# Optimization experiments

Hardware: AMD Instinct MI355X
Metric: run time of the kernel (lower is better)

The kernel has to match this reference:

```python
import jax, jax.numpy as jnp
import numpy as np

DEPTH = 4
H1 = 64
H2 = 16
NF = 5
L = 10.0
K = 4
DIM = 3
N = 2048
NK = N // 4
FEAT = 1 + 2 * NF * DIM  # r scalar + Nf (cos,sin) pairs of dim components


def _tn(k, shape, std=0.01):
    return jax.random.truncated_normal(k, -2.0, 2.0, shape, jnp.float32) * std


def setup_inputs() -> dict:
    key = jax.random.key(0)
    ks = jax.random.split(key, 16)
    comb0 = 3 * DIM + 3 * FEAT   # combine width at depth 0
    combd = 3 * H1 + 3 * H2      # combine width at later depths
    return {
        "sx": jax.random.uniform(ks[0], (N, DIM), jnp.float32) * L,
        "kpoints": jax.random.normal(ks[1], (2 * NK, DIM), jnp.float32),
        "we0": _tn(ks[2], (comb0, H1)), "be0": jnp.zeros((H1,), jnp.float32),
        "we_rest": _tn(ks[3], (DEPTH - 1, combd, H1)), "be_rest": jnp.zeros((DEPTH - 1, H1), jnp.float32),
        "wee0": _tn(ks[4], (FEAT, H2)), "bee0": jnp.zeros((H2,), jnp.float32),
        "wee_rest": _tn(ks[5], (DEPTH - 2, H2, H2)), "bee_rest": jnp.zeros((DEPTH - 2, H2), jnp.float32),
        "wep0": _tn(ks[6], (FEAT, H2)), "bep0": jnp.zeros((H2,), jnp.float32),
        "wep_rest": _tn(ks[7], (DEPTH - 2, H2, H2)), "bep_rest": jnp.zeros((DEPTH - 2, H2), jnp.float32),
        "orb_w_re": _tn(ks[8], (H1, H1)), "orb_w_im": _tn(ks[9], (H1, H1)),
        "orb_b_re": jnp.zeros((H1,), jnp.float32), "orb_b_im": jnp.zeros((H1,), jnp.float32),
        "w_det": _tn(ks[10], (K, H1, H1)),
        "bf_w": _tn(ks[11], (H1, DIM)),
        "mlp_w1": _tn(ks[12], (DIM, H1)), "mlp_b1": jnp.zeros((H1,), jnp.float32),
        "mlp_w2": _tn(ks[13], (H1, K * (NK - 1))), "mlp_b2": jnp.zeros((K * (NK - 1),), jnp.float32),
    }


def _fourier(rij, r):
    # interleaved [r, cos1, sin1, ..., cosNf, sinNf] like the original
    feats = [r[..., None]]
    for k in range(1, NF + 1):
        ang = (2.0 * np.pi * k / L) * rij
        feats.append(jnp.cos(ang))
        feats.append(jnp.sin(ang))
    return jnp.concatenate(feats, axis=-1)


def _combine(e, ee, ep):
    mm = e.shape[0]
    h = mm // 2
    g1a = jnp.broadcast_to(jnp.mean(e[:h], 0, keepdims=True), e.shape)
    g1b = jnp.broadcast_to(jnp.mean(e[h:], 0, keepdims=True), e.shape)
    g2a = jnp.mean(ee[:h], axis=0)
    g2b = jnp.mean(ee[h:], axis=0)
    g3 = jnp.mean(ep, axis=1)
    return jnp.concatenate([e, g1a, g1b, g2a, g2b, g3], axis=1)


def _forward(sx, kpoints, we0, be0, we_rest, be_rest, wee0, bee0, wee_rest, bee_rest,
             wep0, bep0, wep_rest, bep_rest, orb_w_re, orb_w_im, orb_b_re, orb_b_im,
             w_det, bf_w, mlp_w1, mlp_b1, mlp_w2, mlp_b2):
    n, dim = sx.shape
    m, m2 = n // 2, n // 4
    s, x = sx[:m], sx[m:]
    e = jnp.broadcast_to(kpoints[0][None, :], (m, dim))
    # electron-electron pairwise features (m,m,FEAT)
    rij = x[:, None, :] - x[None, :, :]
    eye = jnp.eye(m, dtype=x.dtype)
    r = jnp.linalg.norm(jnp.sin(np.pi * rij / L) + eye[..., None], axis=-1) * (1.0 - eye) * (L / np.pi)
    ee = _fourier(rij, r)
    # electron-proton pairwise features (m,m,FEAT)
    rij = x[:, None, :] - s[None, :, :]
    r = jnp.linalg.norm(jnp.sin(np.pi * rij / L), axis=-1) * (L / np.pi)
    ep = _fourier(rij, r)
    for d in range(DEPTH - 1):
        f = _combine(e, ee, ep)
        We, be = (we0, be0) if d == 0 else (we_rest[d - 1], be_rest[d - 1])
        Wee, bee = (wee0, bee0) if d == 0 else (wee_rest[d - 1], bee_rest[d - 1])
        Wep, bep = (wep0, bep0) if d == 0 else (wep_rest[d - 1], bep_rest[d - 1])
        e_u = jnp.tanh(f @ We + be)
        ee_u = jnp.tanh(ee @ Wee + bee)
        ep_u = jnp.tanh(ep @ Wep + bep)
        e, ee, ep = (e_u + e, ee_u + ee, ep_u + ep) if d > 0 else (e_u, ee_u, ep_u)
    f = _combine(e, ee, ep)
    e = jnp.tanh(f @ we_rest[-1] + be_rest[-1]) + e
    # complex orbitals and geminal pairing matrix phi: (K, m2, m2)
    orb = e.astype(jnp.complex64) @ (orb_w_re + 1j * orb_w_im) + (orb_b_re + 1j * orb_b_im)
    phi = jnp.einsum('ia,kab,jb->kij', orb[:m2], w_det.astype(jnp.complex64), orb[m2:]) + 1.0
    # backflow coordinates and plane-wave determinant factors
    z = e @ bf_w + x
    nk = kpoints.shape[0] // 2
    norm = 1.0 / L ** (dim / 2)
    D_up = norm * jnp.exp(1j * jnp.einsum('kd,id->ki', kpoints[:nk], z[:m2]))  # (nk, m2)
    D_dn = norm * jnp.exp(1j * jnp.einsum('kd,id->ki', kpoints[nk:], z[m2:]))  # (nk, m2)
    h = jnp.tanh(kpoints[0] @ mlp_w1 + mlp_b1)
    fdet = jax.nn.softplus(h @ mlp_w2 + mlp_b2).reshape(K, nk - 1)
    fdet = jnp.concatenate([jnp.ones((K, 1), fdet.dtype), fdet], axis=1)  # (K, nk)
    D = jnp.einsum('ai,ka,aj->kij', D_up, fdet.astype(D_up.dtype), jnp.conj(D_dn))
    # logdet_matmul: stable log of signed sum of K determinants
    phase, logabs = jnp.linalg.slogdet(D * phi)
    maxl = jnp.max(logabs)
    det = jnp.sum(phase * jnp.exp(logabs - maxl))
    return jnp.log(jnp.abs(det)) + maxl + jnp.log(det / jnp.abs(det))


def reference(sx, kpoints, we0, be0, we_rest, be_rest, wee0, bee0, wee_rest, bee_rest,
              wep0, bep0, wep_rest, bep_rest, orb_w_re, orb_w_im, orb_b_re, orb_b_im,
              w_det, bf_w, mlp_w1, mlp_b1, mlp_w2, mlp_b2):
    return _forward(sx, kpoints, we0, be0, we_rest, be_rest, wee0, bee0, wee_rest, bee_rest,
                    wep0, bep0, wep_rest, bep_rest, orb_w_re, orb_w_im, orb_b_re, orb_b_im,
                    w_det, bf_w, mlp_w1, mlp_b1, mlp_w2, mlp_b2)
```

## Files before the change

kernel.cpp:

```cpp
#include <hip/hip_runtime.h>

typedef unsigned int uint;
typedef unsigned short ushort;

#define M1 1024
#define MH 512
#define PI_F 3.14159265358979323846f
#define LBOX 10.0f
#define NB 32

__device__ __forceinline__ float bf2f(ushort h){ return __uint_as_float(((uint)h)<<16); }
__device__ __forceinline__ ushort f2bf(float f){ uint u = __float_as_uint(f); uint r = (u + 0x7fffu + ((u>>16)&1u))>>16; return (ushort)r; }
__device__ __forceinline__ float ftanh(float x){ float e = __expf(2.f*x); return 1.f - 2.f/(e+1.f); }
__device__ __forceinline__ float2 cmul(float2 a, float2 b){ return make_float2(a.x*b.x - a.y*b.y, a.x*b.y + a.y*b.x); }
__device__ __forceinline__ void cfma(float2& c, float2 a, float2 b){
  c.x = fmaf(a.x,b.x,fmaf(-a.y,b.y,c.x));
  c.y = fmaf(a.x,b.y,fmaf(a.y,b.x,c.y));
}

__device__ __forceinline__ void fourier31(float d0, float d1, float d2, bool diag, float f[31]){
  const float k1 = PI_F / LBOX;
  float s[3], c[3];
  __sincosf(k1*d0, &s[0], &c[0]);
  __sincosf(k1*d1, &s[1], &c[1]);
  __sincosf(k1*d2, &s[2], &c[2]);
  float r = diag ? 0.f : (LBOX/PI_F)*sqrtf(s[0]*s[0]+s[1]*s[1]+s[2]*s[2]);
  f[0] = r;
  float cb[3], sb[3], cc[3], sc[3];
  #pragma unroll
  for (int d=0; d<3; ++d){ cb[d] = 1.f - 2.f*s[d]*s[d]; sb[d] = 2.f*s[d]*c[d]; cc[d]=cb[d]; sc[d]=sb[d]; }
  #pragma unroll
  for (int k=0;k<5;++k){
    #pragma unroll
    for (int d=0; d<3; ++d){ f[1+6*k+d] = cc[d]; f[4+6*k+d] = sc[d]; }
    if (k<4){
      #pragma unroll
      for (int d=0; d<3; ++d){
        float nc = cc[d]*cb[d]-sc[d]*sb[d];
        float ns = sc[d]*cb[d]+cc[d]*sb[d];
        cc[d]=nc; sc[d]=ns;
      }
    }
  }
}

__global__ void k_init(float* __restrict__ p, int n, int* __restrict__ rowmap){
  int i = blockIdx.x*256 + threadIdx.x;
  if (i < 2048) rowmap[i] = i & 511;
  for (int q=i; q<n; q+=gridDim.x*256) p[q] = 0.f;
}

__global__ __launch_bounds__(256) void k_pair0(const float* __restrict__ sx, const float* __restrict__ W,
                                               const float* __restrict__ b, ushort* __restrict__ out, int is_ee,
                                               float* __restrict__ gA, float* __restrict__ gB,
                                               float* __restrict__ gH){
  int bx = blockIdx.x;
  int i = bx >> 2;
  int chunk = bx & 3;
  int j = (chunk << 8) + threadIdx.x;
  const float* xs = sx + 3*M1;
  float xi0 = xs[3*i], xi1 = xs[3*i+1], xi2 = xs[3*i+2];
  const float* oth = is_ee ? xs : sx;
  float y0 = oth[3*j], y1 = oth[3*j+1], y2 = oth[3*j+2];
  float f[31];
  fourier31(xi0-y0, xi1-y1, xi2-y2, is_ee && (i==j), f);
  float acc[16];
  #pragma unroll
  for (int o=0;o<16;++o) acc[o] = b[o];
  #pragma unroll
  for (int c=0;c<31;++c){ float fv = f[c];
    #pragma unroll
    for (int o=0;o<16;++o) acc[o] = fmaf(fv, W[c*16+o], acc[o]);
  }
  float hv[16];
  #pragma unroll
  for (int o=0;o<16;++o) hv[o] = ftanh(acc[o]);
  uint u[8];
  #pragma unroll
  for (int h=0;h<8;++h){
    u[h] = (uint)f2bf(hv[2*h]) | ((uint)f2bf(hv[2*h+1])<<16);
  }
  uint4* dst = (uint4*)(out + ((size_t)i*M1 + j)*16);
  dst[0] = make_uint4(u[0],u[1],u[2],u[3]);
  dst[1] = make_uint4(u[4],u[5],u[6],u[7]);
  __shared__ float buf[256*49];
  #pragma unroll
  for (int c=0;c<31;++c) buf[threadIdx.x*49+c] = f[c];
  #pragma unroll
  for (int c=0;c<16;++c) buf[threadIdx.x*49+31+c] = hv[c];
  __syncthreads();
  #pragma unroll
  for (int s=128; s>0; s>>=1){
    if (threadIdx.x < s){
      #pragma unroll
      for (int c=0;c<47;++c) buf[threadIdx.x*49+c] += buf[(threadIdx.x+s)*49+c];
    }
    __syncthreads();
  }
  if (threadIdx.x < 31){
    float* g = (is_ee && chunk >= 2) ? gB : gA;
    atomicAdd(&g[i*31+threadIdx.x], buf[threadIdx.x]);
  } else if (threadIdx.x < 47 && gH){
    atomicAdd(&gH[i*16 + (threadIdx.x-31)], buf[threadIdx.x]);
  }
}

__global__ __launch_bounds__(256) void k_pairU(ushort* __restrict__ ten, const float* __restrict__ W,
                                               const float* __restrict__ b, float* __restrict__ gOut){
  size_t base = ((size_t)blockIdx.x*256 + threadIdx.x)*16;
  uint4 a0 = ((uint4*)(ten+base))[0];
  uint4 a1 = ((uint4*)(ten+base))[1];
  uint uu[8] = {a0.x,a0.y,a0.z,a0.w,a1.x,a1.y,a1.z,a1.w};
  float v[16];
  #pragma unroll
  for (int h=0;h<8;++h){ v[2*h] = bf2f((ushort)(uu[h]&0xffffu)); v[2*h+1] = bf2f((ushort)(uu[h]>>16)); }
  float acc[16];
  #pragma unroll
  for (int o=0;o<16;++o) acc[o] = b[o];
  #pragma unroll
  for (int c=0;c<16;++c){ float fv = v[c];
    #pragma unroll
    for (int o=0;o<16;++o) acc[o] = fmaf(fv, W[c*16+o], acc[o]);
  }
  float nv[16];
  #pragma unroll
  for (int o=0;o<16;++o) nv[o] = ftanh(acc[o]) + v[o];
  uint w[8];
  #pragma unroll
  for (int h=0;h<8;++h){
    w[h] = (uint)f2bf(nv[2*h]) | ((uint)f2bf(nv[2*h+1])<<16);
  }
  ((uint4*)(ten+base))[0] = make_uint4(w[0],w[1],w[2],w[3]);
  ((uint4*)(ten+base))[1] = make_uint4(w[4],w[5],w[6],w[7]);
  __shared__ float buf[256*17];
  if (gOut){
    #pragma unroll
    for (int c=0;c<16;++c) buf[threadIdx.x*17+c] = nv[c];
    __syncthreads();
    #pragma unroll
    for (int s=128; s>0; s>>=1){
      if (threadIdx.x < s){
        #pragma unroll
        for (int c=0;c<16;++c) buf[threadIdx.x*17+c] += buf[(threadIdx.x+s)*17+c];
      }
      __syncthreads();
    }
    if (threadIdx.x < 16){
      int i = blockIdx.x >> 2;
      atomicAdd(&gOut[i*16 + threadIdx.x], buf[threadIdx.x]);
    }
  }
}

__global__ __launch_bounds__(256) void k_gee(const ushort* __restrict__ ten, float* __restrict__ gA, float* __restrict__ gB){
  int jb = blockIdx.x >> 3;
  int ic = blockIdx.x & 7;
  int jl = threadIdx.x & 63;
  int iq = threadIdx.x >> 6;
  int j = jb*64 + jl;
  float acc[16];
  #pragma unroll
  for (int c=0;c<16;++c) acc[c]=0.f;
  for (int s=0;s<32;++s){
    int i = ic*128 + iq + 4*s;
    const uint4* src = (const uint4*)(ten + ((size_t)i*M1 + j)*16);
    uint4 a0 = src[0], a1 = src[1];
    uint uu[8]={a0.x,a0.y,a0.z,a0.w,a1.x,a1.y,a1.z,a1.w};
    #pragma unroll
    for (int h=0;h<8;++h){ acc[2*h]+=bf2f((ushort)(uu[h]&0xffffu)); acc[2*h+1]+=bf2f((ushort)(uu[h]>>16)); }
  }
  __shared__ float red[4][64][16];
  #pragma unroll
  for (int c=0;c<16;++c) red[iq][jl][c]=acc[c];
  __syncthreads();
  if (iq==0){
    float* out = (ic<4)? gA : gB;
    #pragma unroll
    for (int c=0;c<16;++c){
      float t = red[0][jl][c]+red[1][jl][c]+red[2][jl][c]+red[3][jl][c];
      atomicAdd(&out[j*16+c], t);
    }
  }
}

__global__ __launch_bounds__(256) void k_e0(const float* __restrict__ kp, const float* __restrict__ g2a,
    const float* __restrict__ g2b, const float* __restrict__ g3, const float* __restrict__ W,
    const float* __restrict__ b, float* __restrict__ eout, float* __restrict__ g1out){
  int p = blockIdx.x*4 + (threadIdx.x>>6);
  int o = threadIdx.x & 63;
  float acc = b[o];
  #pragma unroll
  for (int d=0; d<3; ++d){
    acc = fmaf(kp[d], W[d*64+o] + W[(d+3)*64+o] + W[(d+6)*64+o], acc);
  }
  const float i512 = 1.f/512.f, i1024 = 1.f/1024.f;
  #pragma unroll
  for (int c=0;c<31;++c){
    float sg = (c!=0 && ((c-1)%6)>=3) ? -i512 : i512;
    acc = fmaf(g2a[p*31+c]*sg, W[(9+c)*64+o], acc);
  }
  #pragma unroll
  for (int c=0;c<31;++c){
    float sg = (c!=0 && ((c-1)%6)>=3) ? -i512 : i512;
    acc = fmaf(g2b[p*31+c]*sg, W[(40+c)*64+o], acc);
  }
  #pragma unroll
  for (int c=0;c<31;++c) acc = fmaf(g3[p*31+c]*i1024, W[(71+c)*64+o], acc);
  float v = ftanh(acc);
  eout[p*64+o] = v;
  atomicAdd(&g1out[(p<MH?0:64)+o], v);
}

__global__ __launch_bounds__(256) void k_eupd(const float* __restrict__ eprev, float* __restrict__ eout,
    const float* __restrict__ W, const float* __restrict__ b, const float* __restrict__ g1in,
    const float* __restrict__ g2a, const float* __restrict__ g2b, const float* __restrict__ g3,
    float* __restrict__ g1out){
  int p = blockIdx.x*4 + (threadIdx.x>>6);
  int o = threadIdx.x & 63;
  const float i512 = 1.f/512.f, i1024 = 1.f/1024.f;
  float acc = b[o];
  #pragma unroll 8
  for (int c=0;c<64;++c) acc = fmaf(eprev[p*64+c], W[c*64+o], acc);
  #pragma unroll 8
  for (int c=0;c<64;++c) acc = fmaf(g1in[c]*i512, W[(64+c)*64+o], acc);
  #pragma unroll 8
  for (int c=0;c<64;++c) acc = fmaf(g1in[64+c]*i512, W[(128+c)*64+o], acc);
  #pragma unroll
  for (int c=0;c<16;++c) acc = fmaf(g2a[p*16+c]*i512, W[(192+c)*64+o], acc);
  #pragma unroll
  for (int c=0;c<16;++c) acc = fmaf(g2b[p*16+c]*i512, W[(208+c)*64+o], acc);
  #pragma unroll
  for (int c=0;c<16;++c) acc = fmaf(g3[p*16+c]*i1024, W[(224+c)*64+o], acc);
  float v = ftanh(acc) + eprev[p*64+o];
  eout[p*64+o] = v;
  if (g1out) atomicAdd(&g1out[(p<MH?0:64)+o], v);
}

__global__ __launch_bounds__(256) void k_orbz(const float* __restrict__ e4, const float* __restrict__ Wre,
    const float* __restrict__ Wim, const float* __restrict__ bre, const float* __restrict__ bim,
    const float* __restrict__ bfw, const float* __restrict__ sx, float* __restrict__ ore,
    float* __restrict__ oim, float* __restrict__ z){
  int p = blockIdx.x*4 + (threadIdx.x>>6);
  int o = threadIdx.x & 63;
  float ar = bre[o], ai = bim[o];
  #pragma unroll 8
  for (int a=0;a<64;++a){ float ev = e4[p*64+a]; ar = fmaf(ev, Wre[a*64+o], ar); ai = fmaf(ev, Wim[a*64+o], ai); }
  ore[p*64+o]=ar; oim[p*64+o]=ai;
  if (o<3){
    float zz = sx[(M1+p)*3+o];
    for (int a=0;a<64;++a) zz = fmaf(e4[p*64+a], bfw[a*3+o], zz);
    z[p*3+o]=zz;
  }
}

__global__ __launch_bounds__(256) void k_fdet(const float* __restrict__ kp, const float* __restrict__ w1,
    const float* __restrict__ b1, const float* __restrict__ w2, const float* __restrict__ b2,
    float* __restrict__ fdet){
  __shared__ float hs[64];
  int tid = threadIdx.x;
  if (tid < 64){
    float acc = b1[tid];
    for (int d=0;d<3;++d) acc = fmaf(kp[d], w1[d*64+tid], acc);
    hs[tid] = ftanh(acc);
  }
  __syncthreads();
  int c = blockIdx.x*256 + tid;
  if (c < 2044){
    float acc = b2[c];
    #pragma unroll 8
    for (int o=0;o<64;++o) acc = fmaf(hs[o], w2[o*2044+c], acc);
    float sp = (acc > 20.f) ? acc : log1pf(__expf(acc));
    int kk = c / 511, idx = c % 511;
    fdet[kk*512 + 1 + idx] = sp;
  }
  if (blockIdx.x == 0 && tid < 4) fdet[tid*512] = 1.f;
}

__global__ __launch_bounds__(256) void k_uv(const float* __restrict__ kp, const float* __restrict__ z,
                                            float2* __restrict__ U, float2* __restrict__ V){
  int gid = blockIdx.x*256 + threadIdx.x;
  int sel = gid >> 18;
  int rem = gid & 262143;
  int a = rem >> 9;
  int col = rem & 511;
  const float nrm = 0.031622776601683794f;
  const float* kr = kp + (sel ? (512+a)*3 : a*3);
  const float* zr = z + (sel ? (512+col)*3 : col*3);
  float th = kr[0]*zr[0] + kr[1]*zr[1] + kr[2]*zr[2];
  float s, c; __sincosf(th, &s, &c);
  float2 v = make_float2(nrm*c, nrm*s);
  if (sel) V[a*512+col] = v; else U[a*512+col] = v;
}

__global__ __launch_bounds__(256) void k_T(const float* __restrict__ ore, const float* __restrict__ oim,
                                           const float* __restrict__ wdet, float2* __restrict__ T){
  int k = blockIdx.x >> 7;
  int iblk = blockIdx.x & 127;
  int i = iblk*4 + (threadIdx.x>>6);
  int bc = threadIdx.x & 63;
  __shared__ float wd[4096];
  for (int t = threadIdx.x; t < 4096; t += 256) wd[t] = wdet[k*4096 + t];
  __syncthreads();
  float ar=0.f, ai=0.f;
  #pragma unroll 8
  for (int a=0;a<64;++a){
    float w = wd[a*64+bc];
    ar = fmaf(ore[i*64+a], w, ar);
    ai = fmaf(oim[i*64+a], w, ai);
  }
  T[((size_t)k*512 + i)*64 + bc] = make_float2(ar, ai);
}

__global__ __launch_bounds__(256) void k_M(const float2* __restrict__ U, const float2* __restrict__ V,
    const float* __restrict__ fdet, const float2* __restrict__ T, const float* __restrict__ ore,
    const float* __restrict__ oim, float2* __restrict__ Mb){
  __shared__ float2 As[16*66];
  __shared__ float2 Bs[16*66];
  int k = blockIdx.z;
  int ib = blockIdx.y * 64, jb = blockIdx.x * 64;
  int tid = threadIdx.x;
  int ti = (tid >> 4) * 4;
  int tj = (tid & 15) * 4;
  const float* fk = fdet + k*512;
  float2 acc[4][4];
  #pragma unroll
  for (int a=0;a<4;++a){
    #pragma unroll
    for (int b=0;b<4;++b) acc[a][b] = make_float2(0.f,0.f);
  }
  for (int a0=0; a0<512; a0+=16){
    #pragma unroll
    for (int s=0;s<4;++s){
      int t = tid + s*256;
      int aa = t >> 6, il = t & 63;
      int a = a0 + aa;
      float fv = fk[a];
      float2 u = U[a*512 + ib + il];
      As[aa*66+il] = make_float2(u.x*fv, u.y*fv);
      float2 v = V[a*512 + jb + il];
      Bs[aa*66+il] = make_float2(v.x, -v.y);
    }
    __syncthreads();
    #pragma unroll
    for (int aa=0;aa<16;++aa){
      float2 Av[4], Bv[4];
      #pragma unroll
      for (int q=0;q<4;++q){ Av[q] = As[aa*66+ti+q]; Bv[q] = Bs[aa*66+tj+q]; }
      #pragma unroll
      for (int qi=0;qi<4;++qi){
        #pragma unroll
        for (int qj=0;qj<4;++qj) cfma(acc[qi][qj], Av[qi], Bv[qj]);
      }
    }
    __syncthreads();
  }
  float2 ph[4][4];
  #pragma unroll
  for (int a=0;a<4;++a){
    #pragma unroll
    for (int b=0;b<4;++b) ph[a][b] = make_float2(1.f,0.f);
  }
  for (int b0=0; b0<64; b0+=16){
    #pragma unroll
    for (int s=0;s<4;++s){
      int t = tid + s*256;
      int aa = t >> 6, il = t & 63;
      As[aa*66+il] = T[((size_t)k*512 + ib + il)*64 + b0 + aa];
      int oidx = (512 + jb + il)*64 + b0 + aa;
      Bs[aa*66+il] = make_float2(ore[oidx], oim[oidx]);
    }
    __syncthreads();
    #pragma unroll
    for (int aa=0;aa<16;++aa){
      float2 Av[4], Bv[4];
      #pragma unroll
      for (int q=0;q<4;++q){ Av[q] = As[aa*66+ti+q]; Bv[q] = Bs[aa*66+tj+q]; }
      #pragma unroll
      for (int qi=0;qi<4;++qi){
        #pragma unroll
        for (int qj=0;qj<4;++qj) cfma(ph[qi][qj], Av[qi], Bv[qj]);
      }
    }
    __syncthreads();
  }
  #pragma unroll
  for (int qi=0;qi<4;++qi){
    size_t ro = ((size_t)k*512 + ib + ti + qi)*512 + jb + tj;
    #pragma unroll
    for (int qj=0;qj<4;++qj) Mb[ro+qj] = cmul(acc[qi][qj], ph[qi][qj]);
  }
}

__global__ __launch_bounds__(512)
void k_panel(float2* __restrict__ Mb, float2* __restrict__ LinvG,
             int* __restrict__ rowmap, int* __restrict__ swapc, int col0){
  int k = blockIdx.x;
  float2* Mk = Mb + (size_t)k*512*512;
  int R = 512 - col0;
  int R64 = R < 64 ? R : 64;
  int rl = threadIdx.x;
  bool active = rl < R;
  int wv = rl >> 6;
  __shared__ float2 mir[64*33];
  __shared__ float2 Us[NB*33];
  __shared__ float2 dinv[NB];
  __shared__ float2 Ls[NB*NB];
  __shared__ float2 Yv[NB*NB];
  __shared__ int winslot[NB];
  __shared__ int newposS[64];
  int rm_orig = active ? rowmap[k*512 + col0 + rl] : 0;
  float2 X[NB];
  if (rl >= 64 && active){
    const float4* rp = (const float4*)(Mk + (size_t)rm_orig*512 + col0);
    #pragma unroll
    for (int q=0;q<NB/2;++q){ float4 v = rp[q]; X[2*q]=make_float2(v.x,v.y); X[2*q+1]=make_float2(v.z,v.w); }
  }
  if (wv == 0){
    if (rl < R64){
      const float4* rp = (const float4*)(Mk + (size_t)rm_orig*512 + col0);
      #pragma unroll
      for (int q=0;q<NB/2;++q){
        float4 v = rp[q];
        mir[rl*33+2*q]   = make_float2(v.x,v.y);
        mir[rl*33+2*q+1] = make_float2(v.z,v.w);
      }
    }
    bool done = false;
    int winpos = 0;
    for (int cc=0; cc<NB; ++cc){
      bool cand = (rl < R64) && !done;
      float2 cv = make_float2(0.f,0.f);
      if (cand) cv = mir[rl*33+cc];
      float val = cand ? fmaf(cv.x,cv.x,cv.y*cv.y) : -1.f;
      int idx = rl;
      #pragma unroll
      for (int off=32; off>0; off>>=1){
        float ov = __shfl_xor(val, off);
        int   oi = __shfl_xor(idx, off);
        if (ov > val || (ov == val && oi < idx)){ val = ov; idx = oi; }
      }
      int p = idx;
      if (rl == 0) winslot[cc] = p;
      if (rl == p){ done = true; winpos = cc; }
      float2 dg = mir[p*33+cc];
      float dn = 1.f/fmaf(dg.x,dg.x,dg.y*dg.y);
      float2 inv = make_float2(dg.x*dn, -dg.y*dn);
      if (cand && rl != p){
        float2 l = cmul(cv, inv);
        mir[rl*33+cc] = l;
        for (int j=cc+1; j<NB; ++j){
          float2 pr = mir[p*33+j];
          float2 xv = mir[rl*33+j];
          xv.x = fmaf(-l.x, pr.x, fmaf( l.y, pr.y, xv.x));
          xv.y = fmaf(-l.x, pr.y, fmaf(-l.y, pr.x, xv.y));
          mir[rl*33+j] = xv;
        }
      }
    }
    unsigned long long nwmask = __ballot(rl < R64 && !done);
    int np = 0;
    if (rl < R64){
      np = done ? winpos : (NB + (int)__popcll(nwmask & ((1ull<<rl)-1ull)));
      newposS[rl] = np;
      rowmap[k*512 + col0 + np] = rm_orig;
      float4* wp = (float4*)(Mk + (size_t)rm_orig*512 + col0);
      #pragma unroll
      for (int q=0;q<NB/2;++q){
        float2 a = mir[rl*33+2*q], bq = mir[rl*33+2*q+1];
        wp[q] = make_float4(a.x,a.y,bq.x,bq.y);
      }
    }
    {
      int cnt = 0;
      for (int t=0;t<R64;++t){
        int nt = newposS[t];
        if (rl < R64 && t > rl && nt < np) cnt++;
      }
      #pragma unroll
      for (int off=32; off>0; off>>=1) cnt += __shfl_xor(cnt, off);
      if (rl == 0) swapc[k] += cnt;
    }
    if (rl < NB){
      int ws = winslot[rl];
      #pragma unroll
      for (int j=0;j<NB;++j){
        float2 v = mir[ws*33+j];
        Us[rl*33+j] = v;
        float2 lv;
        if      (j <  rl) lv = v;
        else if (j == rl) lv = make_float2(1.f,0.f);
        else              lv = make_float2(0.f,0.f);
        Ls[rl*NB+j] = lv;
      }
      float2 d = Us[rl*33+rl];
      float dn = 1.f/fmaf(d.x,d.x,d.y*d.y);
      dinv[rl] = make_float2(d.x*dn, -d.y*dn);
    }
  }
  __syncthreads();
  if (rl >= 64 && active){
    #pragma unroll
    for (int j=0;j<NB;++j){
      float2 t = X[j];
      #pragma unroll
      for (int q=0;q<NB;++q){
        if (q < j){
          float2 u = Us[q*33+j];
          t.x = fmaf(-X[q].x, u.x, fmaf( X[q].y, u.y, t.x));
          t.y = fmaf(-X[q].x, u.y, fmaf(-X[q].y, u.x, t.y));
        }
      }
      X[j] = cmul(t, dinv[j]);
    }
    float4* wp = (float4*)(Mk + (size_t)rm_orig*512 + col0);
    #pragma unroll
    for (int q=0;q<NB/2;++q) wp[q] = make_float4(X[2*q].x,X[2*q].y,X[2*q+1].x,X[2*q+1].y);
  }
  if (rl < NB){
    for (int i=0;i<NB;++i){
      float2 acc = (i==rl)? make_float2(1.f,0.f) : make_float2(0.f,0.f);
      for (int q=rl; q<i; ++q){
        float2 lv = Ls[i*NB+q];
        float2 yv = Yv[q*NB+rl];
        acc.x = fmaf(-lv.x, yv.x, fmaf( lv.y, yv.y, acc.x));
        acc.y = fmaf(-lv.x, yv.y, fmaf(-lv.y, yv.x, acc.y));
      }
      Yv[i*NB+rl] = acc;
    }
  }
  __syncthreads();
  {
    float4* dst = (float4*)(LinvG + (size_t)k*(NB*NB));
    const float4* src = (const float4*)Yv;
    for (int q=rl; q<NB*NB/2; q+=blockDim.x) dst[q] = src[q];
  }
}

__global__ __launch_bounds__(256) void k_gemm(float2* __restrict__ Mb, const float2* __restrict__ LinvG,
                                              const int* __restrict__ rowmap, int col0){
  int k = blockIdx.z;
  float2* Mk = Mb + (size_t)k*512*512;
  int e0 = col0 + NB;
  int r0 = e0 + blockIdx.x*32;
  int j0c = e0 + blockIdx.y*32;
  int tid = threadIdx.x;
  int jl = tid & 31, rg = tid >> 5;
  __shared__ float2 As[NB*33];
  __shared__ float2 Bs[NB*33];
  __shared__ float2 Av[NB*33];
  __shared__ float2 Li[NB*NB];
  __shared__ int prA[32];
  __shared__ int prB[NB];
  if (tid < 32) prA[tid] = rowmap[k*512 + r0 + tid];
  else if (tid < 64) prB[tid-32] = rowmap[k*512 + col0 + (tid-32)];
  {
    const float4* src = (const float4*)(LinvG + (size_t)k*(NB*NB));
    float4* dst = (float4*)Li;
    for (int q=tid; q<NB*NB/2; q+=256) dst[q] = src[q];
  }
  __syncthreads();
  #pragma unroll
  for (int s=0;s<4;++s){
    int a = rg + 8*s;
    Av[a*33 + jl] = Mk[(size_t)prB[a]*512 + j0c + jl];
  }
  for (int t=tid; t<1024; t+=256){
    int rl = t >> 5, kk = t & 31;
    As[kk*33+rl] = Mk[(size_t)prA[rl]*512 + col0 + kk];
  }
  __syncthreads();
  #pragma unroll
  for (int s=0;s<4;++s){
    int m = rg + 8*s;
    float2 acc = make_float2(0.f,0.f);
    #pragma unroll 8
    for (int a=0;a<NB;++a) cfma(acc, Li[m*NB+a], Av[a*33+jl]);
    Bs[m*33+jl] = acc;
  }
  __syncthreads();
  int i0 = (tid >> 4)*2, j0 = (tid & 15)*2;
  float2 a00={0,0},a01={0,0},a10={0,0},a11={0,0};
  #pragma unroll 16
  for (int kk=0;kk<NB;++kk){
    float2 A0 = As[kk*33+i0], A1 = As[kk*33+i0+1];
    float2 B0 = Bs[kk*33+j0], B1 = Bs[kk*33+j0+1];
    cfma(a00,A0,B0); cfma(a01,A0,B1); cfma(a10,A1,B0); cfma(a11,A1,B1);
  }
  size_t ro0 = (size_t)prA[i0]*512 + j0c + j0;
  size_t ro1 = (size_t)prA[i0+1]*512 + j0c + j0;
  float2 c0 = Mk[ro0];   c0.x-=a00.x; c0.y-=a00.y; Mk[ro0]=c0;
  float2 c1 = Mk[ro0+1]; c1.x-=a01.x; c1.y-=a01.y; Mk[ro0+1]=c1;
  float2 c2 = Mk[ro1];   c2.x-=a10.x; c2.y-=a10.y; Mk[ro1]=c2;
  float2 c3 = Mk[ro1+1]; c3.x-=a11.x; c3.y-=a11.y; Mk[ro1+1]=c3;
}

__global__ void k_det(const float2* __restrict__ Mb, const int* __restrict__ rowmap,
                      const int* __restrict__ swapc, float* __restrict__ out, int out_size){
  int tid = threadIdx.x;
  int k = tid >> 6, lane = tid & 63;
  const float2* Mk = Mb + (size_t)k*512*512;
  double la = 0.0, ang = 0.0;
  for (int q=0;q<8;++q){
    int i = lane*8 + q;
    int pr = rowmap[k*512 + i];
    float2 u = Mk[(size_t)pr*512+i];
    double re = (double)u.x, im = (double)u.y;
    la += 0.5*log(re*re + im*im);
    ang += atan2(im, re);
  }
  #pragma unroll
  for (int off=32; off>0; off>>=1){
    la += __shfl_down(la, off);
    ang += __shfl_down(ang, off);
  }
  __shared__ double las[4], angs[4];
  if (lane==0){
    las[k] = la;
    angs[k] = ang + 3.14159265358979323846*(double)(swapc[k] & 1);
  }
  __syncthreads();
  if (tid==0){
    double mx = las[0];
    for (int q=1;q<4;++q) mx = fmax(mx, las[q]);
    double sre=0.0, sim=0.0;
    for (int q=0;q<4;++q){
      double w = exp(las[q]-mx);
      sre += w*cos(angs[q]);
      sim += w*sin(angs[q]);
    }
    double mag = sqrt(sre*sre+sim*sim);
    out[0] = (float)(log(mag)+mx);
    if (out_size > 1) out[1] = (float)atan2(sim, sre);
    for (int q=2;q<out_size;++q) out[q] = 0.f;
  }
}

extern "C" void kernel_launch(void* const* d_in, const int* in_sizes, int n_in,
                              void* d_out, int out_size, void* d_ws, size_t ws_size,
                              hipStream_t stream){
  const float* sx   = (const float*)d_in[0];
  const float* kp   = (const float*)d_in[1];
  const float* we0  = (const float*)d_in[2];
  const float* be0  = (const float*)d_in[3];
  const float* weR  = (const float*)d_in[4];
  const float* beR  = (const float*)d_in[5];
  const float* wee0 = (const float*)d_in[6];
  const float* bee0 = (const float*)d_in[7];
  const float* weeR = (const float*)d_in[8];
  const float* beeR = (const float*)d_in[9];
  const float* wep0 = (const float*)d_in[10];
  const float* bep0 = (const float*)d_in[11];
  const float* wepR = (const float*)d_in[12];
  const float* bepR = (const float*)d_in[13];
  const float* owre = (const float*)d_in[14];
  const float* owim = (const float*)d_in[15];
  const float* obre = (const float*)d_in[16];
  const float* obim = (const float*)d_in[17];
  const float* wdet = (const float*)d_in[18];
  const float* bfw  = (const float*)d_in[19];
  const float* mw1  = (const float*)d_in[20];
  const float* mb1  = (const float*)d_in[21];
  const float* mw2  = (const float*)d_in[22];
  const float* mb2  = (const float*)d_in[23];

  char* ws = (char*)d_ws;
  size_t off = 0;
  auto alloc = [&](size_t bytes)->char*{
    char* p = ws + off;
    off = (off + bytes + 255) & ~(size_t)255;
    return p;
  };
  ushort* ee   = (ushort*)alloc(33554432);
  ushort* ep   = (ushort*)alloc(33554432);
  float2* Mb   = (float2*)alloc(8388608);
  float2* U    = (float2*)alloc(2097152);
  float2* V    = (float2*)alloc(2097152);
  float2* T    = (float2*)alloc(1048576);
  float*  eS   = (float*)alloc(1048576);
  float*  ore  = (float*)alloc(262144);
  float*  oim  = (float*)alloc(262144);
  float*  z    = (float*)alloc(12288);
  float*  fdet = (float*)alloc(8192);
  float2* Linv = (float2*)alloc(131072);
  int*    rowmap = (int*)alloc(8192);
  char*   zst  = ws + off;
  float*  g2a0 = (float*)alloc(126976);
  float*  g2b0 = (float*)alloc(126976);
  float*  g30  = (float*)alloc(126976);
  float*  geeA = (float*)alloc(196608);
  float*  geeB = (float*)alloc(196608);
  float*  gep  = (float*)alloc(196608);
  float*  g1s  = (float*)alloc(1536);
  int*    swpc = (int*)alloc(16);
  int zn = (int)(((char*)(swpc+4) - zst)/4);

  float* e1 = eS;           float* e2 = eS + 65536;
  float* e3 = eS + 131072;  float* e4 = eS + 196608;
  float* geeA1 = geeA;      float* geeA2 = geeA+16384; float* geeA3 = geeA+32768;
  float* geeB1 = geeB;      float* geeB2 = geeB+16384; float* geeB3 = geeB+32768;
  float* gep1  = gep;       float* gep2  = gep+16384;  float* gep3  = gep+32768;
  float* g1s1 = g1s; float* g1s2 = g1s+128; float* g1s3 = g1s+256;

  k_init<<<256,256,0,stream>>>((float*)zst, zn, rowmap);
  k_pair0<<<4096,256,0,stream>>>(sx, wee0, bee0, ee, 1, g2a0, g2b0, nullptr);
  k_pair0<<<4096,256,0,stream>>>(sx, wep0, bep0, ep, 0, g30, g30, gep1);
  k_e0<<<256,256,0,stream>>>(kp, g2a0, g2b0, g30, we0, be0, e1, g1s1);
  k_gee<<<128,256,0,stream>>>(ee, geeA1, geeB1);
  k_eupd<<<256,256,0,stream>>>(e1, e2, weR, beR, g1s1, geeA1, geeB1, gep1, g1s2);
  k_pairU<<<4096,256,0,stream>>>(ee, weeR, beeR, nullptr);
  k_pairU<<<4096,256,0,stream>>>(ep, wepR, bepR, gep2);
  k_gee<<<128,256,0,stream>>>(ee, geeA2, geeB2);
  k_eupd<<<256,256,0,stream>>>(e2, e3, weR+240*64, beR+64, g1s2, geeA2, geeB2, gep2, g1s3);
  k_pairU<<<4096,256,0,stream>>>(ee, weeR+256, beeR+16, nullptr);
  k_pairU<<<4096,256,0,stream>>>(ep, wepR+256, bepR+16, gep3);
  k_gee<<<128,256,0,stream>>>(ee, geeA3, geeB3);
  k_eupd<<<256,256,0,stream>>>(e3, e4, weR+2*240*64, beR+128, g1s3, geeA3, geeB3, gep3, nullptr);
  k_orbz<<<256,256,0,stream>>>(e4, owre, owim, obre, obim, bfw, sx, ore, oim, z);
  k_fdet<<<8,256,0,stream>>>(kp, mw1, mb1, mw2, mb2, fdet);
  k_uv<<<2048,256,0,stream>>>(kp, z, U, V);
  k_T<<<512,256,0,stream>>>(ore, oim, wdet, T);
  k_M<<<dim3(8,8,4),256,0,stream>>>(U, V, fdet, T, ore, oim, Mb);
  for (int tpan=0;tpan<16;++tpan){
    int col0 = tpan*NB;
    int R = 512 - col0;
    int Rpad = (R + 63) & ~63;
    k_panel<<<4, Rpad, 0, stream>>>(Mb, Linv, rowmap, swpc, col0);
    if (tpan < 15){
      int nch = 15 - tpan;
      k_gemm<<<dim3(nch,nch,4),256,0,stream>>>(Mb, Linv, rowmap, col0);
    }
  }
  k_det<<<1,256,0,stream>>>(Mb, rowmap, swpc, (float*)d_out, out_size);
  (void)in_sizes; (void)n_in; (void)ws_size;
}
```

Baseline: 1.894 ms.

## Fuse pair-stream layers, merge small setup kernels, retile k_M for more blocks

The ep stream's three layers are fused into k_pair0, so ep is never written to memory, and the ee and ep pair kernels run as one launch. The ee updates for layers 1-2 and their column-sum reductions are computed on the fly in k_eeL12 from the layer-0 tensor, without rewriting it in place. k_uv, k_T and k_fdet are merged into one launch, and k_M is retiled to 32x64 tiles so it launches 512 blocks instead of 256. This removes several full passes over the large bf16 pair tensors and a number of launches. In exchange it adds register pressure and redundant recomputation per consumer.

```diff
diff --git a/kernel.cpp b/kernel.cpp
--- a/kernel.cpp
+++ b/kernel.cpp
@@ -50,13 +50,19 @@
   for (int q=i; q<n; q+=gridDim.x*256) p[q] = 0.f;
 }
 
-__global__ __launch_bounds__(256) void k_pair0(const float* __restrict__ sx, const float* __restrict__ W,
-                                               const float* __restrict__ b, ushort* __restrict__ out, int is_ee,
-                                               float* __restrict__ gA, float* __restrict__ gB,
-                                               float* __restrict__ gH){
+__global__ __launch_bounds__(256) void k_pair0(const float* __restrict__ sx,
+    const float* __restrict__ Wee, const float* __restrict__ bee,
+    const float* __restrict__ Wep, const float* __restrict__ bep,
+    const float* __restrict__ W1ep, const float* __restrict__ b1ep,
+    const float* __restrict__ W2ep, const float* __restrict__ b2ep,
+    ushort* __restrict__ ee, float* __restrict__ g2a, float* __restrict__ g2b,
+    float* __restrict__ g3, float* __restrict__ gep1, float* __restrict__ gep2,
+    float* __restrict__ gep3){
   int bx = blockIdx.x;
-  int i = bx >> 2;
-  int chunk = bx & 3;
+  bool is_ee = bx < 4096;
+  int bb = is_ee ? bx : bx - 4096;
+  int i = bb >> 2;
+  int chunk = bb & 3;
   int j = (chunk << 8) + threadIdx.x;
   const float* xs = sx + 3*M1;
   float xi0 = xs[3*i], xi1 = xs[3*i+1], xi2 = xs[3*i+2];
@@ -64,6 +70,8 @@
   float y0 = oth[3*j], y1 = oth[3*j+1], y2 = oth[3*j+2];
   float f[31];
   fourier31(xi0-y0, xi1-y1, xi2-y2, is_ee && (i==j), f);
+  const float* W = is_ee ? Wee : Wep;
+  const float* b = is_ee ? bee : bep;
   float acc[16];
   #pragma unroll
   for (int o=0;o<16;++o) acc[o] = b[o];
@@ -75,14 +83,14 @@
   float hv[16];
   #pragma unroll
   for (int o=0;o<16;++o) hv[o] = ftanh(acc[o]);
-  uint u[8];
-  #pragma unroll
-  for (int h=0;h<8;++h){
-    u[h] = (uint)f2bf(hv[2*h]) | ((uint)f2bf(hv[2*h+1])<<16);
-  }
-  uint4* dst = (uint4*)(out + ((size_t)i*M1 + j)*16);
-  dst[0] = make_uint4(u[0],u[1],u[2],u[3]);
-  dst[1] = make_uint4(u[4],u[5],u[6],u[7]);
+  if (is_ee){
+    uint u[8];
+    #pragma unroll
+    for (int h=0;h<8;++h) u[h] = (uint)f2bf(hv[2*h]) | ((uint)f2bf(hv[2*h+1])<<16);
+    uint4* dst = (uint4*)(ee + ((size_t)i*M1 + j)*16);
+    dst[0] = make_uint4(u[0],u[1],u[2],u[3]);
+    dst[1] = make_uint4(u[4],u[5],u[6],u[7]);
+  }
   __shared__ float buf[256*49];
   #pragma unroll
   for (int c=0;c<31;++c) buf[threadIdx.x*49+c] = f[c];
@@ -98,88 +106,136 @@
     __syncthreads();
   }
   if (threadIdx.x < 31){
-    float* g = (is_ee && chunk >= 2) ? gB : gA;
+    float* g = is_ee ? ((chunk >= 2) ? g2b : g2a) : g3;
     atomicAdd(&g[i*31+threadIdx.x], buf[threadIdx.x]);
-  } else if (threadIdx.x < 47 && gH){
-    atomicAdd(&gH[i*16 + (threadIdx.x-31)], buf[threadIdx.x]);
-  }
-}
-
-__global__ __launch_bounds__(256) void k_pairU(ushort* __restrict__ ten, const float* __restrict__ W,
-                                               const float* __restrict__ b, float* __restrict__ gOut){
-  size_t base = ((size_t)blockIdx.x*256 + threadIdx.x)*16;
-  uint4 a0 = ((uint4*)(ten+base))[0];
-  uint4 a1 = ((uint4*)(ten+base))[1];
-  uint uu[8] = {a0.x,a0.y,a0.z,a0.w,a1.x,a1.y,a1.z,a1.w};
-  float v[16];
-  #pragma unroll
-  for (int h=0;h<8;++h){ v[2*h] = bf2f((ushort)(uu[h]&0xffffu)); v[2*h+1] = bf2f((ushort)(uu[h]>>16)); }
-  float acc[16];
-  #pragma unroll
-  for (int o=0;o<16;++o) acc[o] = b[o];
-  #pragma unroll
-  for (int c=0;c<16;++c){ float fv = v[c];
-    #pragma unroll
-    for (int o=0;o<16;++o) acc[o] = fmaf(fv, W[c*16+o], acc[o]);
-  }
-  float nv[16];
-  #pragma unroll
-  for (int o=0;o<16;++o) nv[o] = ftanh(acc[o]) + v[o];
-  uint w[8];
-  #pragma unroll
-  for (int h=0;h<8;++h){
-    w[h] = (uint)f2bf(nv[2*h]) | ((uint)f2bf(nv[2*h+1])<<16);
-  }
-  ((uint4*)(ten+base))[0] = make_uint4(w[0],w[1],w[2],w[3]);
-  ((uint4*)(ten+base))[1] = make_uint4(w[4],w[5],w[6],w[7]);
-  __shared__ float buf[256*17];
-  if (gOut){
-    #pragma unroll
-    for (int c=0;c<16;++c) buf[threadIdx.x*17+c] = nv[c];
+  } else if (threadIdx.x < 47 && !is_ee){
+    atomicAdd(&gep1[i*16 + (threadIdx.x-31)], buf[threadIdx.x]);
+  }
+  if (!is_ee){
+    float v1[16];
+    #pragma unroll
+    for (int o=0;o<16;++o) acc[o] = b1ep[o];
+    #pragma unroll
+    for (int c=0;c<16;++c){ float fv = hv[c];
+      #pragma unroll
+      for (int o=0;o<16;++o) acc[o] = fmaf(fv, W1ep[c*16+o], acc[o]);
+    }
+    #pragma unroll
+    for (int o=0;o<16;++o) v1[o] = ftanh(acc[o]) + hv[o];
+    float v2[16];
+    #pragma unroll
+    for (int o=0;o<16;++o) acc[o] = b2ep[o];
+    #pragma unroll
+    for (int c=0;c<16;++c){ float fv = v1[c];
+      #pragma unroll
+      for (int o=0;o<16;++o) acc[o] = fmaf(fv, W2ep[c*16+o], acc[o]);
+    }
+    #pragma unroll
+    for (int o=0;o<16;++o) v2[o] = ftanh(acc[o]) + v1[o];
+    __syncthreads();
+    #pragma unroll
+    for (int c=0;c<16;++c){ buf[threadIdx.x*49+c] = v1[c]; buf[threadIdx.x*49+16+c] = v2[c]; }
     __syncthreads();
     #pragma unroll
     for (int s=128; s>0; s>>=1){
       if (threadIdx.x < s){
         #pragma unroll
-        for (int c=0;c<16;++c) buf[threadIdx.x*17+c] += buf[(threadIdx.x+s)*17+c];
+        for (int c=0;c<32;++c) buf[threadIdx.x*49+c] += buf[(threadIdx.x+s)*49+c];
       }
       __syncthreads();
     }
-    if (threadIdx.x < 16){
-      int i = blockIdx.x >> 2;
-      atomicAdd(&gOut[i*16 + threadIdx.x], buf[threadIdx.x]);
-    }
-  }
-}
-
-__global__ __launch_bounds__(256) void k_gee(const ushort* __restrict__ ten, float* __restrict__ gA, float* __restrict__ gB){
-  int jb = blockIdx.x >> 3;
-  int ic = blockIdx.x & 7;
+    if (threadIdx.x < 16) atomicAdd(&gep2[i*16+threadIdx.x], buf[threadIdx.x]);
+    else if (threadIdx.x < 32) atomicAdd(&gep3[i*16+(threadIdx.x-16)], buf[threadIdx.x]);
+  }
+}
+
+__global__ __launch_bounds__(256) void k_eeL12(const ushort* __restrict__ ten,
+    const float* __restrict__ W1, const float* __restrict__ b1,
+    const float* __restrict__ W2, const float* __restrict__ b2,
+    float* __restrict__ gA1, float* __restrict__ gB1,
+    float* __restrict__ gA2, float* __restrict__ gB2,
+    float* __restrict__ gA3, float* __restrict__ gB3){
+  int jb = (blockIdx.x & 15) * 64;
+  int ic = blockIdx.x >> 4;
   int jl = threadIdx.x & 63;
   int iq = threadIdx.x >> 6;
-  int j = jb*64 + jl;
-  float acc[16];
-  #pragma unroll
-  for (int c=0;c<16;++c) acc[c]=0.f;
-  for (int s=0;s<32;++s){
-    int i = ic*128 + iq + 4*s;
+  int j = jb + jl;
+  __shared__ float Ws[544];
+  for (int t=threadIdx.x; t<544; t+=256){
+    float v;
+    if      (t < 256) v = W1[t];
+    else if (t < 272) v = b1[t-256];
+    else if (t < 528) v = W2[t-272];
+    else              v = b2[t-528];
+    Ws[t] = v;
+  }
+  __syncthreads();
+  float s0[16], s1[16], s2[16];
+  #pragma unroll
+  for (int c=0;c<16;++c){ s0[c]=0.f; s1[c]=0.f; s2[c]=0.f; }
+  for (int s=0;s<8;++s){
+    int i = ic*32 + iq*8 + s;
     const uint4* src = (const uint4*)(ten + ((size_t)i*M1 + j)*16);
     uint4 a0 = src[0], a1 = src[1];
     uint uu[8]={a0.x,a0.y,a0.z,a0.w,a1.x,a1.y,a1.z,a1.w};
-    #pragma unroll
-    for (int h=0;h<8;++h){ acc[2*h]+=bf2f((ushort)(uu[h]&0xffffu)); acc[2*h+1]+=bf2f((ushort)(uu[h]>>16)); }
+    float v0[16];
+    #pragma unroll
+    for (int h=0;h<8;++h){ v0[2*h] = bf2f((ushort)(uu[h]&0xffffu)); v0[2*h+1] = bf2f((ushort)(uu[h]>>16)); }
+    float ac[16], v1[16], v2[16];
+    #pragma unroll
+    for (int o=0;o<16;++o) ac[o] = Ws[256+o];
+    #pragma unroll
+    for (int c=0;c<16;++c){ float fv = v0[c];
+      #pragma unroll
+      for (int o=0;o<16;++o) ac[o] = fmaf(fv, Ws[c*16+o], ac[o]);
+    }
+    #pragma unroll
+    for (int o=0;o<16;++o) v1[o] = ftanh(ac[o]) + v0[o];
+    #pragma unroll
+    for (int o=0;o<16;++o) ac[o] = Ws[528+o];
+    #pragma unroll
+    for (int c=0;c<16;++c){ float fv = v1[c];
+      #pragma unroll
+      for (int o=0;o<16;++o) ac[o] = fmaf(fv, Ws[272+c*16+o], ac[o]);
+    }
+    #pragma unroll
+    for (int o=0;o<16;++o) v2[o] = ftanh(ac[o]) + v1[o];
+    #pragma unroll
+    for (int c=0;c<16;++c){ s0[c]+=v0[c]; s1[c]+=v1[c]; s2[c]+=v2[c]; }
   }
   __shared__ float red[4][64][16];
-  #pragma unroll
-  for (int c=0;c<16;++c) red[iq][jl][c]=acc[c];
-  __syncthreads();
-  if (iq==0){
-    float* out = (ic<4)? gA : gB;
-    #pragma unroll
-    for (int c=0;c<16;++c){
-      float t = red[0][jl][c]+red[1][jl][c]+red[2][jl][c]+red[3][jl][c];
-      atomicAdd(&out[j*16+c], t);
-    }
+  bool loA = (ic < 16);
+  #pragma unroll
+  for (int c=0;c<16;++c) red[iq][jl][c] = s0[c];
+  __syncthreads();
+  #pragma unroll
+  for (int q=0;q<4;++q){
+    int p = threadIdx.x + 256*q;
+    int jj = p >> 4, c = p & 15;
+    float t = red[0][jj][c]+red[1][jj][c]+red[2][jj][c]+red[3][jj][c];
+    atomicAdd(&(loA? gA1 : gB1)[(jb+jj)*16+c], t);
+  }
+  __syncthreads();
+  #pragma unroll
+  for (int c=0;c<16;++c) red[iq][jl][c] = s1[c];
+  __syncthreads();
+  #pragma unroll
+  for (int q=0;q<4;++q){
+    int p = threadIdx.x + 256*q;
+    int jj = p >> 4, c = p & 15;
+    float t = red[0][jj][c]+red[1][jj][c]+red[2][jj][c]+red[3][jj][c];
+    atomicAdd(&(loA? gA2 : gB2)[(jb+jj)*16+c], t);
+  }
+  __syncthreads();
+  #pragma unroll
+  for (int c=0;c<16;++c) red[iq][jl][c] = s2[c];
+  __syncthreads();
+  #pragma unroll
+  for (int q=0;q<4;++q){
+    int p = threadIdx.x + 256*q;
+    int jj = p >> 4, c = p & 15;
+    float t = red[0][jj][c]+red[1][jj][c]+red[2][jj][c]+red[3][jj][c];
+    atomicAdd(&(loA? gA3 : gB3)[(jb+jj)*16+c], t);
   }
 }
 
@@ -253,141 +309,144 @@
   }
 }
 
-__global__ __launch_bounds__(256) void k_fdet(const float* __restrict__ kp, const float* __restrict__ w1,
-    const float* __restrict__ b1, const float* __restrict__ w2, const float* __restrict__ b2,
-    float* __restrict__ fdet){
-  __shared__ float hs[64];
+__global__ __launch_bounds__(256) void k_uvTf(const float* __restrict__ kp, const float* __restrict__ z,
+    const float* __restrict__ ore, const float* __restrict__ oim, const float* __restrict__ wdet,
+    const float* __restrict__ w1, const float* __restrict__ b1, const float* __restrict__ w2,
+    const float* __restrict__ b2, float2* __restrict__ U, float2* __restrict__ V,
+    float2* __restrict__ T, float* __restrict__ fdet){
+  __shared__ float sh[4096];
+  int bx = blockIdx.x;
   int tid = threadIdx.x;
-  if (tid < 64){
-    float acc = b1[tid];
-    for (int d=0;d<3;++d) acc = fmaf(kp[d], w1[d*64+tid], acc);
-    hs[tid] = ftanh(acc);
-  }
-  __syncthreads();
-  int c = blockIdx.x*256 + tid;
-  if (c < 2044){
-    float acc = b2[c];
+  if (bx < 2048){
+    int gid = bx*256 + tid;
+    int sel = gid >> 18;
+    int rem = gid & 262143;
+    int a = rem >> 9;
+    int col = rem & 511;
+    const float nrm = 0.031622776601683794f;
+    const float* kr = kp + (sel ? (512+a)*3 : a*3);
+    const float* zr = z + (sel ? (512+col)*3 : col*3);
+    float th = kr[0]*zr[0] + kr[1]*zr[1] + kr[2]*zr[2];
+    float s, c; __sincosf(th, &s, &c);
+    float2 v = make_float2(nrm*c, nrm*s);
+    if (sel) V[a*512+col] = v; else U[a*512+col] = v;
+  } else if (bx < 2560){
+    int bb = bx - 2048;
+    int k = bb >> 7;
+    int iblk = bb & 127;
+    int i = iblk*4 + (tid>>6);
+    int bc = tid & 63;
+    for (int t = tid; t < 4096; t += 256) sh[t] = wdet[k*4096 + t];
+    __syncthreads();
+    float ar=0.f, ai=0.f;
     #pragma unroll 8
-    for (int o=0;o<64;++o) acc = fmaf(hs[o], w2[o*2044+c], acc);
-    float sp = (acc > 20.f) ? acc : log1pf(__expf(acc));
-    int kk = c / 511, idx = c % 511;
-    fdet[kk*512 + 1 + idx] = sp;
-  }
-  if (blockIdx.x == 0 && tid < 4) fdet[tid*512] = 1.f;
-}
-
-__global__ __launch_bounds__(256) void k_uv(const float* __restrict__ kp, const float* __restrict__ z,
-                                            float2* __restrict__ U, float2* __restrict__ V){
-  int gid = blockIdx.x*256 + threadIdx.x;
-  int sel = gid >> 18;
-  int rem = gid & 262143;
-  int a = rem >> 9;
-  int col = rem & 511;
-  const float nrm = 0.031622776601683794f;
-  const float* kr = kp + (sel ? (512+a)*3 : a*3);
-  const float* zr = z + (sel ? (512+col)*3 : col*3);
-  float th = kr[0]*zr[0] + kr[1]*zr[1] + kr[2]*zr[2];
-  float s, c; __sincosf(th, &s, &c);
-  float2 v = make_float2(nrm*c, nrm*s);
-  if (sel) V[a*512+col] = v; else U[a*512+col] = v;
-}
-
-__global__ __launch_bounds__(256) void k_T(const float* __restrict__ ore, const float* __restrict__ oim,
-                                           const float* __restrict__ wdet, float2* __restrict__ T){
-  int k = blockIdx.x >> 7;
-  int iblk = blockIdx.x & 127;
-  int i = iblk*4 + (threadIdx.x>>6);
-  int bc = threadIdx.x & 63;
-  __shared__ float wd[4096];
-  for (int t = threadIdx.x; t < 4096; t += 256) wd[t] = wdet[k*4096 + t];
-  __syncthreads();
-  float ar=0.f, ai=0.f;
-  #pragma unroll 8
-  for (int a=0;a<64;++a){
-    float w = wd[a*64+bc];
-    ar = fmaf(ore[i*64+a], w, ar);
-    ai = fmaf(oim[i*64+a], w, ai);
-  }
-  T[((size_t)k*512 + i)*64 + bc] = make_float2(ar, ai);
+    for (int a=0;a<64;++a){
+      float w = sh[a*64+bc];
+      ar = fmaf(ore[i*64+a], w, ar);
+      ai = fmaf(oim[i*64+a], w, ai);
+    }
+    T[((size_t)k*512 + i)*64 + bc] = make_float2(ar, ai);
+  } else {
+    int bb = bx - 2560;
+    if (tid < 64){
+      float acc = b1[tid];
+      for (int d=0;d<3;++d) acc = fmaf(kp[d], w1[d*64+tid], acc);
+      sh[tid] = ftanh(acc);
+    }
+    __syncthreads();
+    int c = bb*256 + tid;
+    if (c < 2044){
+      float acc = b2[c];
+      #pragma unroll 8
+      for (int o=0;o<64;++o) acc = fmaf(sh[o], w2[o*2044+c], acc);
+      float sp = (acc > 20.f) ? acc : log1pf(__expf(acc));
+      int kk = c / 511, idx = c % 511;
+      fdet[kk*512 + 1 + idx] = sp;
+    }
+    if (bb == 0 && tid < 4) fdet[tid*512] = 1.f;
+  }
 }
 
 __global__ __launch_bounds__(256) void k_M(const float2* __restrict__ U, const float2* __restrict__ V,
     const float* __restrict__ fdet, const float2* __restrict__ T, const float* __restrict__ ore,
     const float* __restrict__ oim, float2* __restrict__ Mb){
-  __shared__ float2 As[16*66];
+  __shared__ float2 As[16*34];
   __shared__ float2 Bs[16*66];
-  int k = blockIdx.z;
-  int ib = blockIdx.y * 64, jb = blockIdx.x * 64;
+  int bx = blockIdx.x;
+  int k = bx >> 7;
+  int r = bx & 127;
+  int ib = (r >> 3) * 32;
+  int jb = (r & 7) * 64;
   int tid = threadIdx.x;
-  int ti = (tid >> 4) * 4;
-  int tj = (tid & 15) * 4;
+  int ti = (tid >> 4) * 2;
+  int tj = tid & 15;
   const float* fk = fdet + k*512;
-  float2 acc[4][4];
-  #pragma unroll
-  for (int a=0;a<4;++a){
+  float2 acc[2][4];
+  #pragma unroll
+  for (int a=0;a<2;++a){
     #pragma unroll
     for (int b=0;b<4;++b) acc[a][b] = make_float2(0.f,0.f);
   }
   for (int a0=0; a0<512; a0+=16){
-    #pragma unroll
-    for (int s=0;s<4;++s){
-      int t = tid + s*256;
-      int aa = t >> 6, il = t & 63;
-      int a = a0 + aa;
-      float fv = fk[a];
-      float2 u = U[a*512 + ib + il];
-      As[aa*66+il] = make_float2(u.x*fv, u.y*fv);
-      float2 v = V[a*512 + jb + il];
-      Bs[aa*66+il] = make_float2(v.x, -v.y);
-    }
-    __syncthreads();
-    #pragma unroll
-    for (int aa=0;aa<16;++aa){
-      float2 Av[4], Bv[4];
-      #pragma unroll
-      for (int q=0;q<4;++q){ Av[q] = As[aa*66+ti+q]; Bv[q] = Bs[aa*66+tj+q]; }
-      #pragma unroll
-      for (int qi=0;qi<4;++qi){
-        #pragma unroll
-        for (int qj=0;qj<4;++qj) cfma(acc[qi][qj], Av[qi], Bv[qj]);
-      }
-    }
-    __syncthreads();
-  }
-  float2 ph[4][4];
-  #pragma unroll
-  for (int a=0;a<4;++a){
+    for (int t=tid; t<1536; t+=256){
+      if (t < 512){
+        int aa = t >> 5, il = t & 31;
+        int a = a0 + aa;
+        float fv = fk[a];
+        float2 u = U[a*512 + ib + il];
+        As[aa*34+il] = make_float2(u.x*fv, u.y*fv);
+      } else {
+        int tt = t - 512;
+        int aa = tt >> 6, il = tt & 63;
+        float2 v = V[(a0+aa)*512 + jb + il];
+        Bs[aa*66+il] = make_float2(v.x, -v.y);
+      }
+    }
+    __syncthreads();
+    #pragma unroll
+    for (int aa=0; aa<16; ++aa){
+      float2 A0 = As[aa*34+ti], A1 = As[aa*34+ti+1];
+      float2 B0 = Bs[aa*66+tj], B1 = Bs[aa*66+tj+16];
+      float2 B2 = Bs[aa*66+tj+32], B3 = Bs[aa*66+tj+48];
+      cfma(acc[0][0],A0,B0); cfma(acc[0][1],A0,B1); cfma(acc[0][2],A0,B2); cfma(acc[0][3],A0,B3);
+      cfma(acc[1][0],A1,B0); cfma(acc[1][1],A1,B1); cfma(acc[1][2],A1,B2); cfma(acc[1][3],A1,B3);
+    }
+    __syncthreads();
+  }
+  float2 ph[2][4];
+  #pragma unroll
+  for (int a=0;a<2;++a){
     #pragma unroll
     for (int b=0;b<4;++b) ph[a][b] = make_float2(1.f,0.f);
   }
   for (int b0=0; b0<64; b0+=16){
-    #pragma unroll
-    for (int s=0;s<4;++s){
-      int t = tid + s*256;
-      int aa = t >> 6, il = t & 63;
-      As[aa*66+il] = T[((size_t)k*512 + ib + il)*64 + b0 + aa];
-      int oidx = (512 + jb + il)*64 + b0 + aa;
-      Bs[aa*66+il] = make_float2(ore[oidx], oim[oidx]);
-    }
-    __syncthreads();
-    #pragma unroll
-    for (int aa=0;aa<16;++aa){
-      float2 Av[4], Bv[4];
-      #pragma unroll
-      for (int q=0;q<4;++q){ Av[q] = As[aa*66+ti+q]; Bv[q] = Bs[aa*66+tj+q]; }
-      #pragma unroll
-      for (int qi=0;qi<4;++qi){
-        #pragma unroll
-        for (int qj=0;qj<4;++qj) cfma(ph[qi][qj], Av[qi], Bv[qj]);
-      }
-    }
-    __syncthreads();
-  }
-  #pragma unroll
-  for (int qi=0;qi<4;++qi){
-    size_t ro = ((size_t)k*512 + ib + ti + qi)*512 + jb + tj;
-    #pragma unroll
-    for (int qj=0;qj<4;++qj) Mb[ro+qj] = cmul(acc[qi][qj], ph[qi][qj]);
+    for (int t=tid; t<1536; t+=256){
+      if (t < 512){
+        int il = t >> 4, aa = t & 15;
+        As[aa*34+il] = T[((size_t)k*512 + ib + il)*64 + b0 + aa];
+      } else {
+        int tt = t - 512;
+        int il = tt >> 4, aa = tt & 15;
+        int oidx = (512 + jb + il)*64 + b0 + aa;
+        Bs[aa*66+il] = make_float2(ore[oidx], oim[oidx]);
+      }
+    }
+    __syncthreads();
+    #pragma unroll
+    for (int aa=0; aa<16; ++aa){
+      float2 A0 = As[aa*34+ti], A1 = As[aa*34+ti+1];
+      float2 B0 = Bs[aa*66+tj], B1 = Bs[aa*66+tj+16];
+      float2 B2 = Bs[aa*66+tj+32], B3 = Bs[aa*66+tj+48];
+      cfma(ph[0][0],A0,B0); cfma(ph[0][1],A0,B1); cfma(ph[0][2],A0,B2); cfma(ph[0][3],A0,B3);
+      cfma(ph[1][0],A1,B0); cfma(ph[1][1],A1,B1); cfma(ph[1][2],A1,B2); cfma(ph[1][3],A1,B3);
+    }
+    __syncthreads();
+  }
+  #pragma unroll
+  for (int qi=0;qi<2;++qi){
+    size_t ro = ((size_t)k*512 + ib + ti + qi)*512 + jb;
+    #pragma unroll
+    for (int m=0;m<4;++m) Mb[ro + tj + 16*m] = cmul(acc[qi][m], ph[qi][m]);
   }
 }
 
@@ -700,26 +759,21 @@
   float* geeB1 = geeB;      float* geeB2 = geeB+16384; float* geeB3 = geeB+32768;
   float* gep1  = gep;       float* gep2  = gep+16384;  float* gep3  = gep+32768;
   float* g1s1 = g1s; float* g1s2 = g1s+128; float* g1s3 = g1s+256;
+  (void)ep;
 
   k_init<<<256,256,0,stream>>>((float*)zst, zn, rowmap);
-  k_pair0<<<4096,256,0,stream>>>(sx, wee0, bee0, ee, 1, g2a0, g2b0, nullptr);
-  k_pair0<<<4096,256,0,stream>>>(sx, wep0, bep0, ep, 0, g30, g30, gep1);
+  k_pair0<<<8192,256,0,stream>>>(sx, wee0, bee0, wep0, bep0,
+                                 wepR, bepR, wepR+256, bepR+16,
+                                 ee, g2a0, g2b0, g30, gep1, gep2, gep3);
   k_e0<<<256,256,0,stream>>>(kp, g2a0, g2b0, g30, we0, be0, e1, g1s1);
-  k_gee<<<128,256,0,stream>>>(ee, geeA1, geeB1);
+  k_eeL12<<<512,256,0,stream>>>(ee, weeR, beeR, weeR+256, beeR+16,
+                                geeA1, geeB1, geeA2, geeB2, geeA3, geeB3);
   k_eupd<<<256,256,0,stream>>>(e1, e2, weR, beR, g1s1, geeA1, geeB1, gep1, g1s2);
-  k_pairU<<<4096,256,0,stream>>>(ee, weeR, beeR, nullptr);
-  k_pairU<<<4096,256,0,stream>>>(ep, wepR, bepR, gep2);
-  k_gee<<<128,256,0,stream>>>(ee, geeA2, geeB2);
   k_eupd<<<256,256,0,stream>>>(e2, e3, weR+240*64, beR+64, g1s2, geeA2, geeB2, gep2, g1s3);
-  k_pairU<<<4096,256,0,stream>>>(ee, weeR+256, beeR+16, nullptr);
-  k_pairU<<<4096,256,0,stream>>>(ep, wepR+256, bepR+16, gep3);
-  k_gee<<<128,256,0,stream>>>(ee, geeA3, geeB3);
   k_eupd<<<256,256,0,stream>>>(e3, e4, weR+2*240*64, beR+128, g1s3, geeA3, geeB3, gep3, nullptr);
   k_orbz<<<256,256,0,stream>>>(e4, owre, owim, obre, obim, bfw, sx, ore, oim, z);
-  k_fdet<<<8,256,0,stream>>>(kp, mw1, mb1, mw2, mb2, fdet);
-  k_uv<<<2048,256,0,stream>>>(kp, z, U, V);
-  k_T<<<512,256,0,stream>>>(ore, oim, wdet, T);
-  k_M<<<dim3(8,8,4),256,0,stream>>>(U, V, fdet, T, ore, oim, Mb);
+  k_uvTf<<<2568,256,0,stream>>>(kp, z, ore, oim, wdet, mw1, mb1, mw2, mb2, U, V, T, fdet);
+  k_M<<<512,256,0,stream>>>(U, V, fdet, T, ore, oim, Mb);
   for (int tpan=0;tpan<16;++tpan){
     int col0 = tpan*NB;
     int R = 512 - col0;
```

Result: slower. 1.992 ms (+5.2%).
